# Kernel optimization log

Hardware: AMD Instinct MI355X
Metric: run time of the kernel (lower is better)

## Reference

```python
import jax, jax.numpy as jnp
import numpy as np

B, C, O, K, H, W, CH = 32, 256, 256, 3, 56, 56, 4  # batch, in_planes, out_planes, kernel, spatial, in_chunk
STRIDE, PAD, DIL = 1, 1, 1


def setup_inputs() -> dict:
    key = jax.random.key(0)
    ks = jax.random.split(key, 5)
    gain = np.sqrt(2.0).astype(np.float32)  # calculate_gain('relu')
    x = jax.random.normal(ks[0], (B, C, H, W), jnp.float32)
    # CWFF: fc1 1x1 conv (C->C, no bias), fc2 1x1 conv (C->CH*C, bias)
    fc1_w = jax.random.normal(ks[1], (C, C), jnp.float32) * np.sqrt(2.0 / C).astype(np.float32)  # kaiming fan_out
    fc2_w = jax.random.normal(ks[2], (CH * C, C), jnp.float32) * np.sqrt(2.0 / (CH * C)).astype(np.float32)
    fc2_b = jnp.zeros((CH * C,), jnp.float32)
    cog_weight = jax.random.normal(ks[3], (O, CH, K, K), jnp.float32) * (gain * (CH * K * K) ** -0.5)
    weight = jax.random.normal(ks[4], (O, C, K, K), jnp.float32) * (gain * (C * K * K) ** -0.5)
    return dict(x=x, fc1_w=fc1_w, fc2_w=fc2_w, fc2_b=fc2_b, cog_weight=cog_weight, weight=weight)


def reference(x, fc1_w, fc2_w, fc2_b, cog_weight, weight):
    # CWFF: global avg pool -> 1x1 conv -> relu -> 1x1 conv
    pooled = x.mean(axis=(2, 3))                       # [B, C]
    h = jax.nn.relu(pooled @ fc1_w.T)                  # [B, C]
    kern = h @ fc2_w.T + fc2_b                         # [B, CH*C]
    # torch view(-1, in_chunk, 1, 1): channel dim splits as (c, ch)
    kern = kern.reshape(B, C, CH)                      # [B, C, CH]
    # cognitive weights: conv2d(cog_weight, kernel) == contraction over in_chunk
    cw = jnp.einsum('bct,otij->bocij', kern, cog_weight)   # [B, O, C, K, K]
    dyn_w = jax.nn.sigmoid(cw) * weight[None]               # per-sample kernels [B, O, C, K, K]
    # per-sample conv (groups=B in the original grouped-conv trick)
    def conv1(xi, wi):
        return jax.lax.conv_general_dilated(
            xi[None], wi,
            window_strides=(STRIDE, STRIDE),
            padding=[(PAD, PAD), (PAD, PAD)],
            rhs_dilation=(DIL, DIL))[0]
    return jax.vmap(conv1)(x, dyn_w)                   # [B, O, H, W]
```

## Files before the change

### kernel.cpp

```cpp
#include <hip/hip_runtime.h>

typedef unsigned short u16;
typedef __attribute__((ext_vector_type(4))) float f32x4;
typedef __attribute__((ext_vector_type(8))) short s16x8;
typedef __attribute__((ext_vector_type(4))) unsigned short u16x4;

static __device__ __forceinline__ u16 f2bf(float f) {
    unsigned int x = __float_as_uint(f);
    x += 0x7fffu + ((x >> 16) & 1u);
    return (u16)(x >> 16);
}

__global__ __launch_bounds__(256) void pool_kernel(const float* __restrict__ x,
                                                   float* __restrict__ pooled) {
    int bc = blockIdx.x;
    const float* p = x + (size_t)bc * 3136;
    float s = 0.f;
    for (int i = threadIdx.x; i < 784; i += 256) {
        f32x4 v = *(const f32x4*)(p + i * 4);
        s += v.x + v.y + v.z + v.w;
    }
#pragma unroll
    for (int off = 32; off; off >>= 1) s += __shfl_xor(s, off);
    __shared__ float red[4];
    int lane = threadIdx.x & 63, wave = threadIdx.x >> 6;
    if (lane == 0) red[wave] = s;
    __syncthreads();
    if (threadIdx.x == 0)
        pooled[bc] = (red[0] + red[1] + red[2] + red[3]) * (1.0f / 3136.0f);
}

__global__ __launch_bounds__(256) void fc1_kernel(const float* __restrict__ pooled,
                                                  const float* __restrict__ w,
                                                  float* __restrict__ h) {
    __shared__ float pv[256];
    int b = blockIdx.x >> 6;
    pv[threadIdx.x] = pooled[b * 256 + threadIdx.x];
    __syncthreads();
    int lane = threadIdx.x & 63, wave = threadIdx.x >> 6;
    int i = ((blockIdx.x & 63) << 2) + wave;
    f32x4 v = *(const f32x4*)(w + i * 256 + lane * 4);
    float s = v.x * pv[lane * 4 + 0] + v.y * pv[lane * 4 + 1] +
              v.z * pv[lane * 4 + 2] + v.w * pv[lane * 4 + 3];
#pragma unroll
    for (int off = 32; off; off >>= 1) s += __shfl_xor(s, off);
    if (lane == 0) h[b * 256 + i] = fmaxf(s, 0.f);
}

__global__ __launch_bounds__(256) void fc2_kernel(const float* __restrict__ h,
                                                  const float* __restrict__ w,
                                                  const float* __restrict__ bias,
                                                  float* __restrict__ kern) {
    __shared__ float hv[256];
    int b = blockIdx.x >> 8;
    hv[threadIdx.x] = h[b * 256 + threadIdx.x];
    __syncthreads();
    int lane = threadIdx.x & 63, wave = threadIdx.x >> 6;
    int i = ((blockIdx.x & 255) << 2) + wave;
    f32x4 v = *(const f32x4*)(w + i * 256 + lane * 4);
    float s = v.x * hv[lane * 4 + 0] + v.y * hv[lane * 4 + 1] +
              v.z * hv[lane * 4 + 2] + v.w * hv[lane * 4 + 3];
#pragma unroll
    for (int off = 32; off; off >>= 1) s += __shfl_xor(s, off);
    if (lane == 0) kern[b * 1024 + i] = s + bias[i];
}

__global__ __launch_bounds__(256) void dynw_kernel(const float* __restrict__ kern,
                                                   const float* __restrict__ cogw,
                                                   const float* __restrict__ wgt,
                                                   u16* __restrict__ dynw) {
    __shared__ float wl[2304];
    const int o = blockIdx.x & 255;
    const int bg = blockIdx.x >> 8;
    const int c = threadIdx.x;
    const float* wo = wgt + (size_t)o * 2304;
#pragma unroll
    for (int j = 0; j < 9; ++j)
        wl[j * 256 + c] = wo[j * 256 + c];
    __syncthreads();

    float cg0[9], cg1[9], cg2[9], cg3[9];
#pragma unroll
    for (int p = 0; p < 9; ++p) {
        cg0[p] = cogw[(o * 4 + 0) * 9 + p];
        cg1[p] = cogw[(o * 4 + 1) * 9 + p];
        cg2[p] = cogw[(o * 4 + 2) * 9 + p];
        cg3[p] = cogw[(o * 4 + 3) * 9 + p];
    }
    float w9[9];
#pragma unroll
    for (int p = 0; p < 9; ++p) w9[p] = wl[c * 9 + p];

    for (int b = bg * 8; b < bg * 8 + 8; ++b) {
        f32x4 k4 = *(const f32x4*)(kern + b * 1024 + c * 4);
        u16* dst = dynw + (size_t)(b * 256 + o) * 9 * 256 + c;
#pragma unroll
        for (int p = 0; p < 9; ++p) {
            float cw = k4.x * cg0[p] + k4.y * cg1[p] + k4.z * cg2[p] + k4.w * cg3[p];
            float sg = 1.0f / (1.0f + __expf(-cw));
            dst[p * 256] = f2bf(sg * w9[p]);
        }
    }
}

#define LDSW 40
__global__ __launch_bounds__(256, 2) void conv_kernel(const float* __restrict__ x,
                                                      const u16* __restrict__ dynw,
                                                      float* __restrict__ out) {
    __shared__ u16 lds[2][4 * 58 * LDSW];
    const int tid = threadIdx.x;
    const int wave = tid >> 6, lane = tid & 63;
    const int l15 = lane & 15, quad = lane >> 4;
    const int gid = blockIdx.x;
    const int slot = gid >> 3;
    const int b = (gid & 7) * 4 + slot / 28;
    const int stile = slot % 28;
    const int y0 = stile * 2;

    if (tid < 128) {
        int cg = tid & 7, yy = (tid >> 3) & 3, side = (tid >> 5) & 1, bu = tid >> 6;
        *(u16x4*)&lds[bu][(yy * 58 + (side ? 57 : 0)) * LDSW + cg * 4] =
            (u16x4){0, 0, 0, 0};
    }

    f32x4 acc[4][7];
#pragma unroll
    for (int mf = 0; mf < 4; ++mf)
#pragma unroll
        for (int nf = 0; nf < 7; ++nf) acc[mf][nf] = (f32x4){0.f, 0.f, 0.f, 0.f};

    int bbase[7];
#pragma unroll
    for (int nf = 0; nf < 7; ++nf) {
        int n = nf * 16 + l15;
        int r = (n >= 56) ? 1 : 0;
        int xx = n - 56 * r;
        bbase[nf] = (r * 58 + xx) * LDSW + quad * 8;
    }
    const u16* Abase = dynw + ((size_t)b * 256 + wave * 64 + l15) * 2304 + quad * 8;
    const float* Xb = x + (size_t)b * 256 * 3136;

    int st_goff[7], st_lds[7];
    bool st_ok[7];
#pragma unroll
    for (int it = 0; it < 7; ++it) {
        int i = it * 256 + tid;
        int q = i / 56;
        int xx = i - q * 56;
        int yy = q & 3, cg = q >> 2;
        int yg = y0 - 1 + yy;
        st_ok[it] = (unsigned)yg < 56u;
        st_goff[it] = cg * 4 * 3136 + (st_ok[it] ? yg * 56 + xx : 0);
        st_lds[it] = (yy * 58 + 1 + xx) * LDSW + cg * 4;
    }

    float p0[7], p1[7], p2[7], p3[7];
#define LOADC(cc)                                                         \
    _Pragma("unroll") for (int it = 0; it < 7; ++it) {                    \
        const float* s = Xb + (size_t)(cc) * 32 * 3136 + st_goff[it];     \
        p0[it] = st_ok[it] ? s[0] : 0.f;                                  \
        p1[it] = st_ok[it] ? s[3136] : 0.f;                               \
        p2[it] = st_ok[it] ? s[2 * 3136] : 0.f;                           \
        p3[it] = st_ok[it] ? s[3 * 3136] : 0.f;                           \
    }
#define WRITEC(bu)                                                        \
    _Pragma("unroll") for (int it = 0; it < 7; ++it) {                    \
        u16x4 w = (u16x4){f2bf(p0[it]), f2bf(p1[it]),                     \
                          f2bf(p2[it]), f2bf(p3[it])};                    \
        *(u16x4*)&lds[bu][st_lds[it]] = w;                                \
    }

    LOADC(0)
    WRITEC(0)
    __syncthreads();

    for (int cc = 0; cc < 8; ++cc) {
        const int cur = cc & 1;
        if (cc < 7) { LOADC(cc + 1) }
        const u16* Lb = &lds[cur][0];
#pragma unroll
        for (int p = 0; p < 9; ++p) {
            const int dy = p / 3, dx = p % 3;
            const int tapoff = (dy * 58 + dx) * LDSW;
            s16x8 a0 = *(const s16x8*)(Abase + 0 * 36864 + p * 256 + cc * 32);
            s16x8 a1 = *(const s16x8*)(Abase + 1 * 36864 + p * 256 + cc * 32);
            s16x8 a2 = *(const s16x8*)(Abase + 2 * 36864 + p * 256 + cc * 32);
            s16x8 a3 = *(const s16x8*)(Abase + 3 * 36864 + p * 256 + cc * 32);
#pragma unroll
            for (int nf = 0; nf < 7; ++nf) {
                s16x8 bf = *(const s16x8*)(Lb + bbase[nf] + tapoff);
                acc[0][nf] = __builtin_amdgcn_mfma_f32_16x16x32_bf16(a0, bf, acc[0][nf], 0, 0, 0);
                acc[1][nf] = __builtin_amdgcn_mfma_f32_16x16x32_bf16(a1, bf, acc[1][nf], 0, 0, 0);
                acc[2][nf] = __builtin_amdgcn_mfma_f32_16x16x32_bf16(a2, bf, acc[2][nf], 0, 0, 0);
                acc[3][nf] = __builtin_amdgcn_mfma_f32_16x16x32_bf16(a3, bf, acc[3][nf], 0, 0, 0);
            }
        }
        if (cc < 7) { WRITEC(1 - cur) }
        __syncthreads();
    }

#pragma unroll
    for (int mf = 0; mf < 4; ++mf) {
        int o = wave * 64 + mf * 16 + quad * 4;
        size_t obase = ((size_t)b * 256 + o) * 3136 + (size_t)stile * 112 + l15;
#pragma unroll
        for (int nf = 0; nf < 7; ++nf) {
#pragma unroll
            for (int r = 0; r < 4; ++r)
                out[obase + (size_t)r * 3136 + nf * 16] = acc[mf][nf][r];
        }
    }
}

extern "C" void kernel_launch(void* const* d_in, const int* in_sizes, int n_in,
                              void* d_out, int out_size, void* d_ws, size_t ws_size,
                              hipStream_t stream) {
    const float* x    = (const float*)d_in[0];
    const float* fc1w = (const float*)d_in[1];
    const float* fc2w = (const float*)d_in[2];
    const float* fc2b = (const float*)d_in[3];
    const float* cogw = (const float*)d_in[4];
    const float* wgt  = (const float*)d_in[5];
    float* out = (float*)d_out;

    char* ws = (char*)d_ws;
    float* pooled = (float*)ws;
    float* h      = (float*)(ws + 32768);
    float* kern   = (float*)(ws + 65536);
    u16*   dynw   = (u16*)(ws + 196608);

    pool_kernel<<<8192, 256, 0, stream>>>(x, pooled);
    fc1_kernel<<<2048, 256, 0, stream>>>(pooled, fc1w, h);
    fc2_kernel<<<8192, 256, 0, stream>>>(h, fc2w, fc2b, kern);
    dynw_kernel<<<1024, 256, 0, stream>>>(kern, cogw, wgt, dynw);
    conv_kernel<<<896, 256, 0, stream>>>(x, dynw, out);
}
```

Baseline: 399.1 us.

## Fuse fc1/fc2 into one MLP kernel and vectorize conv input staging

The two fully-connected kernels are merged into one kernel with one block per sample, so the hidden vector stays in shared memory and one launch is dropped. The fused kernel runs only 32 blocks, and each wave loops serially over 64 then 256 output rows, which may lengthen this stage. The conv input staging now reads float4 vectors along x for one channel and writes four scalar bf16 values into LDS. These loads are issued and written straight into the other buffer before the MFMA loop rather than being held in registers until after it. This reduces register pressure and global load count, but it may weaken the overlap of loads with compute and may cause LDS bank conflicts from the scalar 2-byte writes.

```diff
diff --git a/kernel.cpp b/kernel.cpp
--- a/kernel.cpp
+++ b/kernel.cpp
@@ -30,39 +30,36 @@
         pooled[bc] = (red[0] + red[1] + red[2] + red[3]) * (1.0f / 3136.0f);
 }
 
-__global__ __launch_bounds__(256) void fc1_kernel(const float* __restrict__ pooled,
-                                                  const float* __restrict__ w,
-                                                  float* __restrict__ h) {
-    __shared__ float pv[256];
-    int b = blockIdx.x >> 6;
-    pv[threadIdx.x] = pooled[b * 256 + threadIdx.x];
-    __syncthreads();
-    int lane = threadIdx.x & 63, wave = threadIdx.x >> 6;
-    int i = ((blockIdx.x & 63) << 2) + wave;
-    f32x4 v = *(const f32x4*)(w + i * 256 + lane * 4);
-    float s = v.x * pv[lane * 4 + 0] + v.y * pv[lane * 4 + 1] +
-              v.z * pv[lane * 4 + 2] + v.w * pv[lane * 4 + 3];
-#pragma unroll
-    for (int off = 32; off; off >>= 1) s += __shfl_xor(s, off);
-    if (lane == 0) h[b * 256 + i] = fmaxf(s, 0.f);
-}
-
-__global__ __launch_bounds__(256) void fc2_kernel(const float* __restrict__ h,
-                                                  const float* __restrict__ w,
+__global__ __launch_bounds__(256) void mlp_kernel(const float* __restrict__ pooled,
+                                                  const float* __restrict__ w1,
+                                                  const float* __restrict__ w2,
                                                   const float* __restrict__ bias,
                                                   float* __restrict__ kern) {
-    __shared__ float hv[256];
-    int b = blockIdx.x >> 8;
-    hv[threadIdx.x] = h[b * 256 + threadIdx.x];
-    __syncthreads();
-    int lane = threadIdx.x & 63, wave = threadIdx.x >> 6;
-    int i = ((blockIdx.x & 255) << 2) + wave;
-    f32x4 v = *(const f32x4*)(w + i * 256 + lane * 4);
-    float s = v.x * hv[lane * 4 + 0] + v.y * hv[lane * 4 + 1] +
-              v.z * hv[lane * 4 + 2] + v.w * hv[lane * 4 + 3];
-#pragma unroll
-    for (int off = 32; off; off >>= 1) s += __shfl_xor(s, off);
-    if (lane == 0) kern[b * 1024 + i] = s + bias[i];
+    __shared__ float pv[256], hv[256];
+    const int b = blockIdx.x;
+    const int tid = threadIdx.x;
+    const int lane = tid & 63, wave = tid >> 6;
+    pv[tid] = pooled[b * 256 + tid];
+    __syncthreads();
+    for (int k = 0; k < 64; ++k) {
+        int i = wave * 64 + k;
+        f32x4 v = *(const f32x4*)(w1 + (size_t)i * 256 + lane * 4);
+        float s = v.x * pv[lane * 4 + 0] + v.y * pv[lane * 4 + 1] +
+                  v.z * pv[lane * 4 + 2] + v.w * pv[lane * 4 + 3];
+#pragma unroll
+        for (int off = 32; off; off >>= 1) s += __shfl_xor(s, off);
+        if (lane == 0) hv[i] = fmaxf(s, 0.f);
+    }
+    __syncthreads();
+    for (int k = 0; k < 256; ++k) {
+        int i = wave * 256 + k;
+        f32x4 v = *(const f32x4*)(w2 + (size_t)i * 256 + lane * 4);
+        float s = v.x * hv[lane * 4 + 0] + v.y * hv[lane * 4 + 1] +
+                  v.z * hv[lane * 4 + 2] + v.w * hv[lane * 4 + 3];
+#pragma unroll
+        for (int off = 32; off; off >>= 1) s += __shfl_xor(s, off);
+        if (lane == 0) kern[b * 1024 + i] = s + bias[i];
+    }
 }
 
 __global__ __launch_bounds__(256) void dynw_kernel(const float* __restrict__ kern,
@@ -140,43 +137,42 @@
     const u16* Abase = dynw + ((size_t)b * 256 + wave * 64 + l15) * 2304 + quad * 8;
     const float* Xb = x + (size_t)b * 256 * 3136;
 
-    int st_goff[7], st_lds[7];
-    bool st_ok[7];
 #pragma unroll
     for (int it = 0; it < 7; ++it) {
         int i = it * 256 + tid;
-        int q = i / 56;
-        int xx = i - q * 56;
-        int yy = q & 3, cg = q >> 2;
+        int c = i / 56, rem = i % 56;
+        int yy = rem / 14, xg = rem % 14;
         int yg = y0 - 1 + yy;
-        st_ok[it] = (unsigned)yg < 56u;
-        st_goff[it] = cg * 4 * 3136 + (st_ok[it] ? yg * 56 + xx : 0);
-        st_lds[it] = (yy * 58 + 1 + xx) * LDSW + cg * 4;
-    }
-
-    float p0[7], p1[7], p2[7], p3[7];
-#define LOADC(cc)                                                         \
-    _Pragma("unroll") for (int it = 0; it < 7; ++it) {                    \
-        const float* s = Xb + (size_t)(cc) * 32 * 3136 + st_goff[it];     \
-        p0[it] = st_ok[it] ? s[0] : 0.f;                                  \
-        p1[it] = st_ok[it] ? s[3136] : 0.f;                               \
-        p2[it] = st_ok[it] ? s[2 * 3136] : 0.f;                           \
-        p3[it] = st_ok[it] ? s[3 * 3136] : 0.f;                           \
-    }
-#define WRITEC(bu)                                                        \
-    _Pragma("unroll") for (int it = 0; it < 7; ++it) {                    \
-        u16x4 w = (u16x4){f2bf(p0[it]), f2bf(p1[it]),                     \
-                          f2bf(p2[it]), f2bf(p3[it])};                    \
-        *(u16x4*)&lds[bu][st_lds[it]] = w;                                \
-    }
-
-    LOADC(0)
-    WRITEC(0)
+        f32x4 v = (f32x4){0.f, 0.f, 0.f, 0.f};
+        if ((unsigned)yg < 56u)
+            v = *(const f32x4*)(Xb + (size_t)c * 3136 + yg * 56 + xg * 4);
+        int base = (yy * 58 + 1 + xg * 4) * LDSW + c;
+        lds[0][base]            = f2bf(v.x);
+        lds[0][base + LDSW]     = f2bf(v.y);
+        lds[0][base + 2 * LDSW] = f2bf(v.z);
+        lds[0][base + 3 * LDSW] = f2bf(v.w);
+    }
     __syncthreads();
 
     for (int cc = 0; cc < 8; ++cc) {
         const int cur = cc & 1;
-        if (cc < 7) { LOADC(cc + 1) }
+        if (cc < 7) {
+#pragma unroll
+            for (int it = 0; it < 7; ++it) {
+                int i = it * 256 + tid;
+                int c = i / 56, rem = i % 56;
+                int yy = rem / 14, xg = rem % 14;
+                int yg = y0 - 1 + yy;
+                f32x4 v = (f32x4){0.f, 0.f, 0.f, 0.f};
+                if ((unsigned)yg < 56u)
+                    v = *(const f32x4*)(Xb + (size_t)(cc * 32 + 32 + c) * 3136 + yg * 56 + xg * 4);
+                int base = (yy * 58 + 1 + xg * 4) * LDSW + c;
+                lds[1 - cur][base]            = f2bf(v.x);
+                lds[1 - cur][base + LDSW]     = f2bf(v.y);
+                lds[1 - cur][base + 2 * LDSW] = f2bf(v.z);
+                lds[1 - cur][base + 3 * LDSW] = f2bf(v.w);
+            }
+        }
         const u16* Lb = &lds[cur][0];
 #pragma unroll
         for (int p = 0; p < 9; ++p) {
@@ -195,7 +191,6 @@
                 acc[3][nf] = __builtin_amdgcn_mfma_f32_16x16x32_bf16(a3, bf, acc[3][nf], 0, 0, 0);
             }
         }
-        if (cc < 7) { WRITEC(1 - cur) }
         __syncthreads();
     }
 
@@ -225,13 +220,11 @@
 
     char* ws = (char*)d_ws;
     float* pooled = (float*)ws;
-    float* h      = (float*)(ws + 32768);
     float* kern   = (float*)(ws + 65536);
     u16*   dynw   = (u16*)(ws + 196608);
 
     pool_kernel<<<8192, 256, 0, stream>>>(x, pooled);
-    fc1_kernel<<<2048, 256, 0, stream>>>(pooled, fc1w, h);
-    fc2_kernel<<<8192, 256, 0, stream>>>(h, fc2w, fc2b, kern);
+    mlp_kernel<<<32, 256, 0, stream>>>(pooled, fc1w, fc2w, fc2b, kern);
     dynw_kernel<<<1024, 256, 0, stream>>>(kern, cogw, wgt, dynw);
     conv_kernel<<<896, 256, 0, stream>>>(x, dynw, out);
 }
```

After: 564.4 us. +41.4%, slower.
